# Kernel optimization log

Measured on AMD Instinct MI355X. Metric: run time of the kernel, lower is better.

The kernel has to match this reference:

```python
import jax, jax.numpy as jnp
from jax import lax
import numpy as np

N_T = 70            # linspace(0, 60, 70) RK4 grid
STATE_DIM = 12
NOISE_STD = 0.01
T0 = jnp.linspace(0.0, 60.0, N_T)
DEFAULT_TIMES = jnp.array([0, 2, 4, 6, 8, 10, 12, 14, 16, 18, 20, 25, 30, 40, 50, 60], dtype=jnp.float32)
EPORA_DATA = jnp.array([0.01713, 0.145, 0.2442, 0.7659, 1.0, 0.8605, 0.7829, 0.5705,
                        0.6217, 0.331, 0.3388, 0.3116, 0.05062, 0.02504, 0.01163, 0.01163], dtype=jnp.float32)
PARAM_SHIFT = jnp.array([0.5, 0.05, 4.0], dtype=jnp.float32)
PARAM_SCALE = jnp.array([2.5, 0.15, 6.0], dtype=jnp.float32)


def _deriv(x, k1, k2, tau, E):
    # x: [B, 12]; k1,k2,tau: [B]; E: scalar EpoRA(t)
    x1, x2, x3 = x[:, 0], x[:, 1], x[:, 2]
    q1, q2, q3, q4, q5, q6, q7, out = (x[:, 4], x[:, 5], x[:, 6], x[:, 7],
                                       x[:, 8], x[:, 9], x[:, 10], x[:, 11])
    r = 8.0 / tau
    return jnp.stack([
        -k1 * x1 * E + k2 * out,
        -x2 * x2 + k1 * x1 * E,
        -k2 * x3 + x2 * x2,
        -k2 * out + k2 * x3,
        r * (x3 - q1),
        r * (q1 - q2),
        r * (q2 - q3),
        r * (q3 - q4),
        r * (q4 - q5),
        r * (q5 - q6),
        r * (q6 - q7),
        r * (q7 - out),
    ], axis=1)


def _simulate(ps):
    # ps: [B, 3] transformed parameters -> trajectory [N_T, B, 12]
    B = ps.shape[0]
    k1, k2, tau = ps[:, 0], ps[:, 1], ps[:, 2]
    dt = T0[1] - T0[0]
    t_start = T0[:-1]
    # EpoRA is a function of t only: precompute at the 3 RK4 stage times per step
    e_lo = jnp.interp(t_start, DEFAULT_TIMES, EPORA_DATA)
    e_mid = jnp.interp(t_start + 0.5 * dt, DEFAULT_TIMES, EPORA_DATA)
    e_hi = jnp.interp(t_start + dt, DEFAULT_TIMES, EPORA_DATA)
    x0 = jnp.zeros((B, STATE_DIM), dtype=ps.dtype).at[:, 0].set(3.71)

    def step(x, es):
        ea, eb, ec = es
        s1 = _deriv(x, k1, k2, tau, ea)
        s2 = _deriv(x + 0.5 * dt * s1, k1, k2, tau, eb)
        s3 = _deriv(x + 0.5 * dt * s2, k1, k2, tau, eb)
        s4 = _deriv(x + dt * s3, k1, k2, tau, ec)
        xn = x + (dt / 6.0) * (s1 + 2.0 * s2 + 2.0 * s3 + s4)
        return xn, xn

    _, traj = lax.scan(step, x0, (e_lo, e_mid, e_hi))
    return jnp.concatenate([x0[None], traj], axis=0)  # [70, B, 12]


def _forward(parameters, design):
    ps = PARAM_SHIFT + jax.scipy.stats.norm.cdf(parameters) * PARAM_SCALE  # [B,3]
    sol = _simulate(ps)                                   # [70, B, 12]
    y1 = 0.33 * (sol[:, :, 1] + sol[:, :, 2]).T           # [B, 70]
    y2 = 0.26 * (sol[:, :, 0] + sol[:, :, 1] + sol[:, :, 2]).T
    interp = jax.vmap(lambda yb: jnp.interp(design, T0, yb))
    return jnp.concatenate([interp(y1), interp(y2)], axis=1)  # [B, 2*obs_dim]


def setup_inputs() -> dict:
    key = jax.random.key(0)
    k1, k2, k3 = jax.random.split(key, 3)
    B, OBS = 65536, 8
    parameters = jax.random.normal(k1, (B, 3), dtype=jnp.float32)
    design = jnp.sort(60.0 * jax.random.uniform(k2, (OBS,), dtype=jnp.float32))
    noise = jax.random.normal(k3, (B, 2 * OBS), dtype=jnp.float32)
    return {"parameters": parameters, "design": design, "noise": noise}


def reference(parameters, design, noise):
    true_obs = _forward(parameters, design)
    noised_obs = true_obs + NOISE_STD * noise
    return true_obs, noised_obs
```

## Files before the change

### kernel.cpp

```cpp
#include <hip/hip_runtime.h>
#include <math.h>

#define NSTEP 69
#define OBS 8

typedef float f32x2 __attribute__((ext_vector_type(2)));

namespace {

constexpr float kDT = 60.0f / 69.0f;

struct ETab { float lo[NSTEP]; float mid[NSTEP]; float hi[NSTEP]; };

constexpr float interp_e(float t) {
    constexpr float DTm[16] = {0.f,2.f,4.f,6.f,8.f,10.f,12.f,14.f,16.f,18.f,20.f,25.f,30.f,40.f,50.f,60.f};
    constexpr float EP[16]  = {0.01713f,0.145f,0.2442f,0.7659f,1.0f,0.8605f,0.7829f,0.5705f,
                               0.6217f,0.331f,0.3388f,0.3116f,0.05062f,0.02504f,0.01163f,0.01163f};
    if (t >= 60.0f) return EP[15];
    if (t <= 0.0f)  return EP[0];
    int k = 0;
    for (int m = 0; m < 15; m++) if (t >= DTm[m]) k = m;
    float u = (t - DTm[k]) / (DTm[k + 1] - DTm[k]);
    return EP[k] + u * (EP[k + 1] - EP[k]);
}

constexpr ETab make_etab() {
    ETab e{};
    for (int s = 0; s < NSTEP; s++) {
        float t0 = (float)s * kDT;
        e.lo[s]  = interp_e(t0);
        e.mid[s] = interp_e(t0 + 0.5f * kDT);
        e.hi[s]  = interp_e(t0 + kDT);
    }
    return e;
}

}

__device__ constexpr ETab ETAB = make_etab();

struct St { float x0, x1, x2; f32x2 P0, P1, P2, P3; };
struct Dv { float d0, d1, d2; f32x2 D0, D1, D2, D3; };

__device__ __forceinline__ Dv deriv(const St& s, float k1E, float k2, f32x2 r2) {
    Dv d;
    float a  = k1E * s.x0;
    float sq = s.x1 * s.x1;
    d.d0 = fmaf(k2, s.P3.y, -a);
    d.d1 = a - sq;
    d.d2 = fmaf(-k2, s.x2, sq);
    f32x2 s0; s0.x = s.x2; s0.y = s.P3.x;
    d.D0 = r2 * (s0   - s.P0);
    d.D1 = r2 * (s.P0 - s.P1);
    d.D2 = r2 * (s.P1 - s.P2);
    d.D3 = r2 * (s.P2 - s.P3);
    return d;
}

__device__ __forceinline__ St axpy(const St& x, float c, const Dv& d) {
    St y; f32x2 c2 = {c, c};
    y.x0 = fmaf(c, d.d0, x.x0);
    y.x1 = fmaf(c, d.d1, x.x1);
    y.x2 = fmaf(c, d.d2, x.x2);
    y.P0 = c2 * d.D0 + x.P0;
    y.P1 = c2 * d.D1 + x.P1;
    y.P2 = c2 * d.D2 + x.P2;
    y.P3 = c2 * d.D3 + x.P3;
    return y;
}

__global__ __launch_bounds__(256) void stats5_kernel(
    const float* __restrict__ params,
    const float* __restrict__ design,
    const float* __restrict__ noise,
    float* __restrict__ out,
    int B)
{
    int b = blockIdx.x * blockDim.x + threadIdx.x;
    if (b >= B) return;

    int ij[OBS], ij1[OBS]; float wj[OBS], w1j[OBS];
    #pragma unroll
    for (int j = 0; j < OBS; j++) {
        float pos = design[j] * (1.0f / kDT);
        int i = (int)pos;
        i = i < 0 ? 0 : (i > NSTEP - 1 ? NSTEP - 1 : i);
        float w = pos - (float)i;
        ij[j]  = __builtin_amdgcn_readfirstlane(i);
        ij1[j] = ij[j] + 1;
        int wb = __builtin_amdgcn_readfirstlane(__float_as_int(w));
        wj[j]  = __int_as_float(wb);
        w1j[j] = 1.0f - wj[j];
    }

    unsigned long long m_lo = 0ull, m_hi = 0ull;
    #pragma unroll
    for (int j = 0; j < OBS; j++) {
        if (ij[j]  < 64) m_lo |= 1ull << ij[j];  else m_hi |= 1ull << (ij[j]  - 64);
        if (ij1[j] < 64) m_lo |= 1ull << ij1[j]; else m_hi |= 1ull << (ij1[j] - 64);
    }

    float p0 = params[3 * b], p1 = params[3 * b + 1], p2 = params[3 * b + 2];
    const float INV_SQRT2 = 0.7071067811865476f;
    float k1  = fmaf(0.5f * erfcf(-p0 * INV_SQRT2), 2.5f,  0.5f);
    float k2  = fmaf(0.5f * erfcf(-p1 * INV_SQRT2), 0.15f, 0.05f);
    float tau = fmaf(0.5f * erfcf(-p2 * INV_SQRT2), 6.0f,  4.0f);
    float r = 8.0f / tau;
    f32x2 r2 = {r, r};

    float a12[OBS], a0[OBS], b12[OBS], b0[OBS];
    #pragma unroll
    for (int j = 0; j < OBS; j++) { a12[j] = 0.f; a0[j] = 0.f; b12[j] = 0.f; b0[j] = 0.f; }

    St x;
    x.x0 = 3.71f; x.x1 = 0.f; x.x2 = 0.f;
    x.P0 = (f32x2){0.f, 0.f}; x.P1 = x.P0; x.P2 = x.P0; x.P3 = x.P0;

    if (m_lo & 1ull) {
        #pragma unroll
        for (int j = 0; j < OBS; j++)
            if (ij[j] == 0) { a12[j] = 0.f; a0[j] = 3.71f; }
    }

    for (int s = 0; s < NSTEP; s++) {
        float ea = ETAB.lo[s], eb = ETAB.mid[s], ec = ETAB.hi[s];
        float k1a = k1 * ea, k1b = k1 * eb, k1c = k1 * ec;

        Dv d1 = deriv(x, k1a, k2, r2);
        St t  = axpy(x, 0.5f * kDT, d1);
        Dv d2 = deriv(t, k1b, k2, r2);
        t     = axpy(x, 0.5f * kDT, d2);
        Dv d3 = deriv(t, k1b, k2, r2);
        t     = axpy(x, kDT, d3);
        Dv d4 = deriv(t, k1c, k2, r2);

        const float c6 = kDT * (1.0f / 6.0f);
        {
            float u;
            u = fmaf(2.0f, d2.d0 + d3.d0, d1.d0 + d4.d0); x.x0 = fmaf(c6, u, x.x0);
            u = fmaf(2.0f, d2.d1 + d3.d1, d1.d1 + d4.d1); x.x1 = fmaf(c6, u, x.x1);
            u = fmaf(2.0f, d2.d2 + d3.d2, d1.d2 + d4.d2); x.x2 = fmaf(c6, u, x.x2);
            f32x2 two = {2.0f, 2.0f}, c62 = {c6, c6}, v;
            v = two * (d2.D0 + d3.D0) + (d1.D0 + d4.D0); x.P0 = c62 * v + x.P0;
            v = two * (d2.D1 + d3.D1) + (d1.D1 + d4.D1); x.P1 = c62 * v + x.P1;
            v = two * (d2.D2 + d3.D2) + (d1.D2 + d4.D2); x.P2 = c62 * v + x.P2;
            v = two * (d2.D3 + d3.D3) + (d1.D3 + d4.D3); x.P3 = c62 * v + x.P3;
        }

        int ti = s + 1;
        bool any = (ti < 64) ? ((m_lo >> ti) & 1ull) : ((m_hi >> (ti - 64)) & 1ull);
        if (any) {
            float s12 = x.x1 + x.x2;
            #pragma unroll
            for (int j = 0; j < OBS; j++) {
                if (ti == ij[j])  { a12[j] = s12; a0[j] = x.x0; }
                if (ti == ij1[j]) { b12[j] = s12; b0[j] = x.x0; }
            }
        }
    }

    float o1[OBS], o2[OBS];
    #pragma unroll
    for (int j = 0; j < OBS; j++) {
        o1[j] = 0.33f * fmaf(w1j[j], a12[j], wj[j] * b12[j]);
        o2[j] = 0.26f * fmaf(w1j[j], a0[j] + a12[j], wj[j] * (b0[j] + b12[j]));
    }

    long long base = (long long)b * 16;
    long long nb   = (long long)B * 16;
    float4* outv = (float4*)(out + base);
    float4* outn = (float4*)(out + nb + base);
    const float4* nz = (const float4*)(noise + base);

    float4 v0 = make_float4(o1[0], o1[1], o1[2], o1[3]);
    float4 v1 = make_float4(o1[4], o1[5], o1[6], o1[7]);
    float4 v2 = make_float4(o2[0], o2[1], o2[2], o2[3]);
    float4 v3 = make_float4(o2[4], o2[5], o2[6], o2[7]);
    outv[0] = v0; outv[1] = v1; outv[2] = v2; outv[3] = v3;

    float4 n0 = nz[0], n1 = nz[1], n2 = nz[2], n3 = nz[3];
    outn[0] = make_float4(fmaf(0.01f, n0.x, v0.x), fmaf(0.01f, n0.y, v0.y),
                          fmaf(0.01f, n0.z, v0.z), fmaf(0.01f, n0.w, v0.w));
    outn[1] = make_float4(fmaf(0.01f, n1.x, v1.x), fmaf(0.01f, n1.y, v1.y),
                          fmaf(0.01f, n1.z, v1.z), fmaf(0.01f, n1.w, v1.w));
    outn[2] = make_float4(fmaf(0.01f, n2.x, v2.x), fmaf(0.01f, n2.y, v2.y),
                          fmaf(0.01f, n2.z, v2.z), fmaf(0.01f, n2.w, v2.w));
    outn[3] = make_float4(fmaf(0.01f, n3.x, v3.x), fmaf(0.01f, n3.y, v3.y),
                          fmaf(0.01f, n3.z, v3.z), fmaf(0.01f, n3.w, v3.w));
}

extern "C" void kernel_launch(void* const* d_in, const int* in_sizes, int n_in,
                              void* d_out, int out_size, void* d_ws, size_t ws_size,
                              hipStream_t stream) {
    const float* params = (const float*)d_in[0];
    const float* design = (const float*)d_in[1];
    const float* noise  = (const float*)d_in[2];
    float* out = (float*)d_out;
    int B = in_sizes[0] / 3;
    int block = 256;
    int grid = (B + block - 1) / block;
    stats5_kernel<<<grid, block, 0, stream>>>(params, design, noise, out, B);
}
```

Before: 87.97 us.

## Split each RK4 trajectory across two lanes with a shuffled delay-chain boundary

Each batch element is now integrated by a pair of lanes. Both lanes redundantly compute the three reaction states, and each owns half of the eight-stage delay chain. The boundary values (q4 and out) are exchanged with a lane xor-shuffle in every derivative evaluation. This doubles the thread count so a latency-bound serial RK4 kernel runs more waves per CU, and the even and odd lanes split the plain and noised output stores. The cost is redundant scalar work, four shuffles per step, loss of packed f32x2 math, and a loop forced not to unroll.

```diff
diff --git a/kernel.cpp b/kernel.cpp
--- a/kernel.cpp
+++ b/kernel.cpp
@@ -3,8 +3,6 @@
 
 #define NSTEP 69
 #define OBS 8
-
-typedef float f32x2 __attribute__((ext_vector_type(2)));
 
 namespace {
 
@@ -39,33 +37,35 @@
 
 __device__ constexpr ETab ETAB = make_etab();
 
-struct St { float x0, x1, x2; f32x2 P0, P1, P2, P3; };
-struct Dv { float d0, d1, d2; f32x2 D0, D1, D2, D3; };
-
-__device__ __forceinline__ Dv deriv(const St& s, float k1E, float k2, f32x2 r2) {
-    Dv d;
+struct St7 { float x0, x1, x2, c0, c1, c2, c3; };
+struct Dv7 { float d0, d1, d2, e0, e1, e2, e3; };
+
+__device__ __forceinline__ Dv7 deriv(const St7& s, float k1E, float k2, float r, bool hi) {
+    float tp = __shfl_xor(s.c3, 1, 64);
+    float hp = hi ? tp   : s.x2;
+    float ov = hi ? s.c3 : tp;
     float a  = k1E * s.x0;
     float sq = s.x1 * s.x1;
-    d.d0 = fmaf(k2, s.P3.y, -a);
+    Dv7 d;
+    d.d0 = fmaf(k2, ov, -a);
     d.d1 = a - sq;
     d.d2 = fmaf(-k2, s.x2, sq);
-    f32x2 s0; s0.x = s.x2; s0.y = s.P3.x;
-    d.D0 = r2 * (s0   - s.P0);
-    d.D1 = r2 * (s.P0 - s.P1);
-    d.D2 = r2 * (s.P1 - s.P2);
-    d.D3 = r2 * (s.P2 - s.P3);
+    d.e0 = r * (hp   - s.c0);
+    d.e1 = r * (s.c0 - s.c1);
+    d.e2 = r * (s.c1 - s.c2);
+    d.e3 = r * (s.c2 - s.c3);
     return d;
 }
 
-__device__ __forceinline__ St axpy(const St& x, float c, const Dv& d) {
-    St y; f32x2 c2 = {c, c};
+__device__ __forceinline__ St7 axpy(const St7& x, float c, const Dv7& d) {
+    St7 y;
     y.x0 = fmaf(c, d.d0, x.x0);
     y.x1 = fmaf(c, d.d1, x.x1);
     y.x2 = fmaf(c, d.d2, x.x2);
-    y.P0 = c2 * d.D0 + x.P0;
-    y.P1 = c2 * d.D1 + x.P1;
-    y.P2 = c2 * d.D2 + x.P2;
-    y.P3 = c2 * d.D3 + x.P3;
+    y.c0 = fmaf(c, d.e0, x.c0);
+    y.c1 = fmaf(c, d.e1, x.c1);
+    y.c2 = fmaf(c, d.e2, x.c2);
+    y.c3 = fmaf(c, d.e3, x.c3);
     return y;
 }
 
@@ -76,8 +76,10 @@
     float* __restrict__ out,
     int B)
 {
-    int b = blockIdx.x * blockDim.x + threadIdx.x;
-    if (b >= B) return;
+    int t = blockIdx.x * blockDim.x + threadIdx.x;
+    int e = t >> 1;
+    if (e >= B) return;
+    const bool hi = (t & 1);
 
     int ij[OBS], ij1[OBS]; float wj[OBS], w1j[OBS];
     #pragma unroll
@@ -100,21 +102,20 @@
         if (ij1[j] < 64) m_lo |= 1ull << ij1[j]; else m_hi |= 1ull << (ij1[j] - 64);
     }
 
-    float p0 = params[3 * b], p1 = params[3 * b + 1], p2 = params[3 * b + 2];
+    float p0 = params[3 * e], p1 = params[3 * e + 1], p2 = params[3 * e + 2];
     const float INV_SQRT2 = 0.7071067811865476f;
     float k1  = fmaf(0.5f * erfcf(-p0 * INV_SQRT2), 2.5f,  0.5f);
     float k2  = fmaf(0.5f * erfcf(-p1 * INV_SQRT2), 0.15f, 0.05f);
     float tau = fmaf(0.5f * erfcf(-p2 * INV_SQRT2), 6.0f,  4.0f);
     float r = 8.0f / tau;
-    f32x2 r2 = {r, r};
 
     float a12[OBS], a0[OBS], b12[OBS], b0[OBS];
     #pragma unroll
     for (int j = 0; j < OBS; j++) { a12[j] = 0.f; a0[j] = 0.f; b12[j] = 0.f; b0[j] = 0.f; }
 
-    St x;
+    St7 x;
     x.x0 = 3.71f; x.x1 = 0.f; x.x2 = 0.f;
-    x.P0 = (f32x2){0.f, 0.f}; x.P1 = x.P0; x.P2 = x.P0; x.P3 = x.P0;
+    x.c0 = 0.f; x.c1 = 0.f; x.c2 = 0.f; x.c3 = 0.f;
 
     if (m_lo & 1ull) {
         #pragma unroll
@@ -122,17 +123,18 @@
             if (ij[j] == 0) { a12[j] = 0.f; a0[j] = 3.71f; }
     }
 
+    #pragma unroll 1
     for (int s = 0; s < NSTEP; s++) {
         float ea = ETAB.lo[s], eb = ETAB.mid[s], ec = ETAB.hi[s];
         float k1a = k1 * ea, k1b = k1 * eb, k1c = k1 * ec;
 
-        Dv d1 = deriv(x, k1a, k2, r2);
-        St t  = axpy(x, 0.5f * kDT, d1);
-        Dv d2 = deriv(t, k1b, k2, r2);
-        t     = axpy(x, 0.5f * kDT, d2);
-        Dv d3 = deriv(t, k1b, k2, r2);
-        t     = axpy(x, kDT, d3);
-        Dv d4 = deriv(t, k1c, k2, r2);
+        Dv7 d1 = deriv(x, k1a, k2, r, hi);
+        St7 tt = axpy(x, 0.5f * kDT, d1);
+        Dv7 d2 = deriv(tt, k1b, k2, r, hi);
+        tt     = axpy(x, 0.5f * kDT, d2);
+        Dv7 d3 = deriv(tt, k1b, k2, r, hi);
+        tt     = axpy(x, kDT, d3);
+        Dv7 d4 = deriv(tt, k1c, k2, r, hi);
 
         const float c6 = kDT * (1.0f / 6.0f);
         {
@@ -140,16 +142,15 @@
             u = fmaf(2.0f, d2.d0 + d3.d0, d1.d0 + d4.d0); x.x0 = fmaf(c6, u, x.x0);
             u = fmaf(2.0f, d2.d1 + d3.d1, d1.d1 + d4.d1); x.x1 = fmaf(c6, u, x.x1);
             u = fmaf(2.0f, d2.d2 + d3.d2, d1.d2 + d4.d2); x.x2 = fmaf(c6, u, x.x2);
-            f32x2 two = {2.0f, 2.0f}, c62 = {c6, c6}, v;
-            v = two * (d2.D0 + d3.D0) + (d1.D0 + d4.D0); x.P0 = c62 * v + x.P0;
-            v = two * (d2.D1 + d3.D1) + (d1.D1 + d4.D1); x.P1 = c62 * v + x.P1;
-            v = two * (d2.D2 + d3.D2) + (d1.D2 + d4.D2); x.P2 = c62 * v + x.P2;
-            v = two * (d2.D3 + d3.D3) + (d1.D3 + d4.D3); x.P3 = c62 * v + x.P3;
+            u = fmaf(2.0f, d2.e0 + d3.e0, d1.e0 + d4.e0); x.c0 = fmaf(c6, u, x.c0);
+            u = fmaf(2.0f, d2.e1 + d3.e1, d1.e1 + d4.e1); x.c1 = fmaf(c6, u, x.c1);
+            u = fmaf(2.0f, d2.e2 + d3.e2, d1.e2 + d4.e2); x.c2 = fmaf(c6, u, x.c2);
+            u = fmaf(2.0f, d2.e3 + d3.e3, d1.e3 + d4.e3); x.c3 = fmaf(c6, u, x.c3);
         }
 
         int ti = s + 1;
-        bool any = (ti < 64) ? ((m_lo >> ti) & 1ull) : ((m_hi >> (ti - 64)) & 1ull);
-        if (any) {
+        unsigned long long mm = (ti < 64) ? (m_lo >> ti) : (m_hi >> (ti - 64));
+        if (__builtin_expect((int)(mm & 1ull), 0)) {
             float s12 = x.x1 + x.x2;
             #pragma unroll
             for (int j = 0; j < OBS; j++) {
@@ -166,27 +167,30 @@
         o2[j] = 0.26f * fmaf(w1j[j], a0[j] + a12[j], wj[j] * (b0[j] + b12[j]));
     }
 
-    long long base = (long long)b * 16;
-    long long nb   = (long long)B * 16;
-    float4* outv = (float4*)(out + base);
-    float4* outn = (float4*)(out + nb + base);
-    const float4* nz = (const float4*)(noise + base);
-
     float4 v0 = make_float4(o1[0], o1[1], o1[2], o1[3]);
     float4 v1 = make_float4(o1[4], o1[5], o1[6], o1[7]);
     float4 v2 = make_float4(o2[0], o2[1], o2[2], o2[3]);
     float4 v3 = make_float4(o2[4], o2[5], o2[6], o2[7]);
-    outv[0] = v0; outv[1] = v1; outv[2] = v2; outv[3] = v3;
-
-    float4 n0 = nz[0], n1 = nz[1], n2 = nz[2], n3 = nz[3];
-    outn[0] = make_float4(fmaf(0.01f, n0.x, v0.x), fmaf(0.01f, n0.y, v0.y),
-                          fmaf(0.01f, n0.z, v0.z), fmaf(0.01f, n0.w, v0.w));
-    outn[1] = make_float4(fmaf(0.01f, n1.x, v1.x), fmaf(0.01f, n1.y, v1.y),
-                          fmaf(0.01f, n1.z, v1.z), fmaf(0.01f, n1.w, v1.w));
-    outn[2] = make_float4(fmaf(0.01f, n2.x, v2.x), fmaf(0.01f, n2.y, v2.y),
-                          fmaf(0.01f, n2.z, v2.z), fmaf(0.01f, n2.w, v2.w));
-    outn[3] = make_float4(fmaf(0.01f, n3.x, v3.x), fmaf(0.01f, n3.y, v3.y),
-                          fmaf(0.01f, n3.z, v3.z), fmaf(0.01f, n3.w, v3.w));
+
+    long long base = (long long)e * 16;
+    long long nb   = (long long)B * 16;
+
+    if (!hi) {
+        float4* outv = (float4*)(out + base);
+        outv[0] = v0; outv[1] = v1; outv[2] = v2; outv[3] = v3;
+    } else {
+        const float4* nz = (const float4*)(noise + base);
+        float4 n0 = nz[0], n1 = nz[1], n2 = nz[2], n3 = nz[3];
+        float4* outn = (float4*)(out + nb + base);
+        outn[0] = make_float4(fmaf(0.01f, n0.x, v0.x), fmaf(0.01f, n0.y, v0.y),
+                              fmaf(0.01f, n0.z, v0.z), fmaf(0.01f, n0.w, v0.w));
+        outn[1] = make_float4(fmaf(0.01f, n1.x, v1.x), fmaf(0.01f, n1.y, v1.y),
+                              fmaf(0.01f, n1.z, v1.z), fmaf(0.01f, n1.w, v1.w));
+        outn[2] = make_float4(fmaf(0.01f, n2.x, v2.x), fmaf(0.01f, n2.y, v2.y),
+                              fmaf(0.01f, n2.z, v2.z), fmaf(0.01f, n2.w, v2.w));
+        outn[3] = make_float4(fmaf(0.01f, n3.x, v3.x), fmaf(0.01f, n3.y, v3.y),
+                              fmaf(0.01f, n3.z, v3.z), fmaf(0.01f, n3.w, v3.w));
+    }
 }
 
 extern "C" void kernel_launch(void* const* d_in, const int* in_sizes, int n_in,
@@ -197,7 +201,8 @@
     const float* noise  = (const float*)d_in[2];
     float* out = (float*)d_out;
     int B = in_sizes[0] / 3;
+    int threads = 2 * B;
     int block = 256;
-    int grid = (B + block - 1) / block;
+    int grid = (threads + block - 1) / block;
     stats5_kernel<<<grid, block, 0, stream>>>(params, design, noise, out, B);
 }
```

After: 93.90 us. +6.7%, slower.
